# Kernel tuning notes

Measured on AMD Instinct MI355X. Metric: run time of the kernel, lower is better.

The kernel has to match this reference:

```python
import jax, jax.numpy as jnp
import numpy as np

B, D, NB, Z, POOL, C = 16, 2048, 8, 64, 2048, 10
H = 256  # hypernetwork hidden width


def setup_inputs() -> dict:
    key = jax.random.key(0)
    ks = jax.random.split(key, 12)
    s = lambda k, shape, scale=1.0: jax.random.normal(k, shape, dtype=jnp.float32) * scale
    return {
        "features": s(ks[0], (B, D)),
        "seeds": jax.random.randint(ks[1], (B,), 0, POOL),
        "seed_emb": s(ks[2], (POOL, Z)),                 # nn.Embedding weight
        "static_coeffs": s(ks[3], (1, NB)),              # static_accuracy_coeffs
        "hw1": s(ks[4], (Z, H), 1.0 / np.sqrt(Z)),       # hypernetwork Linear 1
        "hb1": jnp.zeros((H,), jnp.float32),
        "hw2": s(ks[5], (H, NB), 1.0 / np.sqrt(H)),      # hypernetwork Linear 2
        "hb2": jnp.zeros((NB,), jnp.float32),
        "wq": s(ks[6], (NB, D, D)),                      # stacked basis_weights_q
        "wk": s(ks[7], (NB, D, D)),
        "wv": s(ks[8], (NB, D, D)),
        "cw": s(ks[9], (D, C), 1.0 / np.sqrt(D)),        # classifier weight (in,out)
        "cb": jnp.zeros((C,), jnp.float32),
    }


def reference(features, seeds, seed_emb, static_coeffs, hw1, hb1, hw2, hb2,
              wq, wk, wv, cw, cb):
    # seed embedding lookup -> hypernetwork -> mixing coefficients
    z = seed_emb[seeds]                                     # [B, Z]
    h = jax.nn.relu(z @ hw1 + hb1)                          # [B, H]
    coeffs_div = jax.nn.softmax(h @ hw2 + hb2, axis=1)      # [B, NB]
    coeffs_acc = jax.nn.softmax(static_coeffs, axis=1)      # [1, NB]
    coeffs = coeffs_acc + coeffs_div                        # [B, NB]

    # Fused basis-weight synthesis + projection:
    # q_b = sum_i coeffs[b,i] * (features[b] @ W_i)  -- never materialize [B,D,D]
    q = jnp.einsum('bi,bj,ijk->bk', coeffs, features, wq)   # [B, D]
    k = jnp.einsum('bi,bj,ijk->bk', coeffs, features, wk)
    v = jnp.einsum('bi,bj,ijk->bk', coeffs, features, wv)

    # seq_len = 1 self-attention
    scores = jnp.einsum('bk,bk->b', q, k) / jnp.sqrt(jnp.float32(D))
    attn_map = jax.nn.softmax(scores.reshape(B, 1, 1), axis=-1)  # [B,1,1] (== ones)
    pooled = attn_map[:, 0] * v                              # [B, D]

    logits = pooled @ cw + cb                                # [B, C]
    return logits, attn_map
```

## Files before the change

kernel.cpp:

```cpp
#include <hip/hip_runtime.h>
#include <math.h>

#define D    2048
#define NB   8
#define BSZ  16
#define ZZ   64
#define HH   256
#define CC   10
#define NPAIR (NB * D)
#define GSPLIT 64
#define KC     8

__global__ __launch_bounds__(256) void k_mt(
    const float* __restrict__ feat, const int* __restrict__ seeds,
    const float* __restrict__ semb, const float* __restrict__ statc,
    const float* __restrict__ hw1, const float* __restrict__ hb1,
    const float* __restrict__ hw2, const float* __restrict__ hb2,
    float* __restrict__ Mt, float* __restrict__ out)
{
    int t = threadIdx.x, blk = blockIdx.x;
    __shared__ float zs[BSZ][ZZ];
    __shared__ float hs[BSZ][HH];
    __shared__ float lgs[BSZ][NB];
    __shared__ float cshs[BSZ][NB];

    for (int e = t; e < BSZ * ZZ; e += 256) {
        int b = e >> 6, u = e & (ZZ - 1);
        zs[b][u] = semb[seeds[b] * ZZ + u];
    }
    __syncthreads();

    {
        float acc[BSZ];
        float bias = hb1[t];
        #pragma unroll
        for (int b = 0; b < BSZ; ++b) acc[b] = bias;
        #pragma unroll 4
        for (int u = 0; u < ZZ; ++u) {
            float w = hw1[u * HH + t];
            #pragma unroll
            for (int b = 0; b < BSZ; ++b) acc[b] = fmaf(zs[b][u], w, acc[b]);
        }
        #pragma unroll
        for (int b = 0; b < BSZ; ++b) hs[b][t] = fmaxf(acc[b], 0.f);
    }
    __syncthreads();

    if (t < BSZ * NB) {
        int b = t >> 3, c = t & (NB - 1);
        float s = hb2[c];
        #pragma unroll 4
        for (int u = 0; u < HH; ++u) s = fmaf(hs[b][u], hw2[u * NB + c], s);
        lgs[b][c] = s;
    }
    __syncthreads();

    if (t < BSZ) {
        int b = t;
        float m = lgs[b][0];
        #pragma unroll
        for (int i = 1; i < NB; ++i) m = fmaxf(m, lgs[b][i]);
        float e[NB], s = 0.f;
        #pragma unroll
        for (int i = 0; i < NB; ++i) { e[i] = expf(lgs[b][i] - m); s += e[i]; }
        float m2 = statc[0];
        #pragma unroll
        for (int i = 1; i < NB; ++i) m2 = fmaxf(m2, statc[i]);
        float e2[NB], s2 = 0.f;
        #pragma unroll
        for (int i = 0; i < NB; ++i) { e2[i] = expf(statc[i] - m2); s2 += e2[i]; }
        #pragma unroll
        for (int i = 0; i < NB; ++i) cshs[b][i] = e[i] / s + e2[i] / s2;
        if (blk == 0) out[BSZ * CC + b] = 1.0f;
    }
    __syncthreads();

    int p = blk * 256 + t;
    int i = blk >> 3;
    int j = (blk & 7) * 256 + t;
    float vals[BSZ];
    #pragma unroll
    for (int b = 0; b < BSZ; ++b) vals[b] = cshs[b][i] * feat[b * D + j];
    float4* dst = reinterpret_cast<float4*>(Mt + (size_t)p * BSZ);
    dst[0] = make_float4(vals[0],  vals[1],  vals[2],  vals[3]);
    dst[1] = make_float4(vals[4],  vals[5],  vals[6],  vals[7]);
    dst[2] = make_float4(vals[8],  vals[9],  vals[10], vals[11]);
    dst[3] = make_float4(vals[12], vals[13], vals[14], vals[15]);
}

__global__ __launch_bounds__(512, 4) void k_partial(
    const float* __restrict__ wv, const float* __restrict__ Mt,
    float* __restrict__ part)
{
    int kc   = blockIdx.x;
    int g    = blockIdx.y;
    int t    = threadIdx.x;
    int wave = t >> 6;
    int lane = t & 63;
    int col  = kc * 256 + lane * 4;

    __shared__ float mt[256 * BSZ];
    __shared__ float4 sh[4][8][64];

    {
        const float4* src = reinterpret_cast<const float4*>(Mt + (size_t)g * 256 * BSZ);
        float4* dst = reinterpret_cast<float4*>(mt);
        dst[t]       = src[t];
        dst[t + 512] = src[t + 512];
    }
    __syncthreads();

    float4 acc[BSZ];
    #pragma unroll
    for (int b = 0; b < BSZ; ++b) acc[b] = make_float4(0.f, 0.f, 0.f, 0.f);

    int pair0 = wave * 32;
    const float* wp = wv + ((size_t)(g * 256 + pair0)) * D + col;

    #pragma unroll 4
    for (int it = 0; it < 32; ++it) {
        const float4 w = *reinterpret_cast<const float4*>(wp + (size_t)it * D);
        const float4* ap4 = reinterpret_cast<const float4*>(mt + (pair0 + it) * BSZ);
        float4 a0 = ap4[0], a1 = ap4[1], a2 = ap4[2], a3 = ap4[3];
        const float am[BSZ] = {a0.x, a0.y, a0.z, a0.w, a1.x, a1.y, a1.z, a1.w,
                               a2.x, a2.y, a2.z, a2.w, a3.x, a3.y, a3.z, a3.w};
        #pragma unroll
        for (int b = 0; b < BSZ; ++b) {
            float a = am[b];
            acc[b].x = fmaf(a, w.x, acc[b].x);
            acc[b].y = fmaf(a, w.y, acc[b].y);
            acc[b].z = fmaf(a, w.z, acc[b].z);
            acc[b].w = fmaf(a, w.w, acc[b].w);
        }
    }

    for (int round = 0; round < 4; ++round) {
        #pragma unroll
        for (int bb = 0; bb < 4; ++bb)
            sh[bb][wave][lane] = acc[round * 4 + bb];
        __syncthreads();
        if (wave < 4) {
            float4 s = sh[wave][0][lane];
            #pragma unroll
            for (int sw = 1; sw < 8; ++sw) {
                float4 x = sh[wave][sw][lane];
                s.x += x.x; s.y += x.y; s.z += x.z; s.w += x.w;
            }
            int b = round * 4 + wave;
            *reinterpret_cast<float4*>(part + ((size_t)(g * BSZ + b)) * D + col) = s;
        }
        __syncthreads();
    }
}

__global__ __launch_bounds__(256) void k_reduce(
    const float* __restrict__ part, float* __restrict__ v)
{
    int idx = blockIdx.x * 256 + threadIdx.x;
    int b = idx >> 11;
    int k = idx & (D - 1);
    float s[16];
    #pragma unroll
    for (int r = 0; r < 16; ++r) s[r] = 0.f;
    for (int g = 0; g < GSPLIT; g += 16) {
        #pragma unroll
        for (int r = 0; r < 16; ++r)
            s[r] += part[((size_t)((g + r) * BSZ + b)) * D + k];
    }
    float t0 = ((s[0] + s[1]) + (s[2] + s[3])) + ((s[4] + s[5]) + (s[6] + s[7]));
    float t1 = ((s[8] + s[9]) + (s[10] + s[11])) + ((s[12] + s[13]) + (s[14] + s[15]));
    v[idx] = t0 + t1;
}

__global__ __launch_bounds__(256) void k_cls(
    const float* __restrict__ v, const float* __restrict__ cw,
    const float* __restrict__ cb, float* __restrict__ out)
{
    int b = blockIdx.x, t = threadIdx.x;
    int wave = t >> 6, lane = t & 63;
    float lacc[CC];
    #pragma unroll
    for (int c = 0; c < CC; ++c) lacc[c] = 0.f;
    for (int k = t; k < D; k += 256) {
        float vv = v[b * D + k];
        const float* cwr = cw + k * CC;
        #pragma unroll
        for (int c = 0; c < CC; ++c) lacc[c] = fmaf(vv, cwr[c], lacc[c]);
    }
    __shared__ float sred[4][CC];
    #pragma unroll
    for (int c = 0; c < CC; ++c) {
        float val = lacc[c];
        for (int off = 32; off > 0; off >>= 1) val += __shfl_down(val, off);
        if (lane == 0) sred[wave][c] = val;
    }
    __syncthreads();
    if (t < CC)
        out[b * CC + t] = sred[0][t] + sred[1][t] + sred[2][t] + sred[3][t] + cb[t];
}

extern "C" void kernel_launch(void* const* d_in, const int* in_sizes, int n_in,
                              void* d_out, int out_size, void* d_ws, size_t ws_size,
                              hipStream_t stream)
{
    const float* feat  = (const float*)d_in[0];
    const int*   seeds = (const int*)  d_in[1];
    const float* semb  = (const float*)d_in[2];
    const float* statc = (const float*)d_in[3];
    const float* hw1   = (const float*)d_in[4];
    const float* hb1   = (const float*)d_in[5];
    const float* hw2   = (const float*)d_in[6];
    const float* hb2   = (const float*)d_in[7];
    const float* wv    = (const float*)d_in[10];
    const float* cw    = (const float*)d_in[11];
    const float* cb    = (const float*)d_in[12];
    float* out = (float*)d_out;

    float* Mt   = (float*)d_ws;
    float* part = Mt + (size_t)NPAIR * BSZ;
    float* v    = part + (size_t)GSPLIT * BSZ * D;

    hipLaunchKernelGGL(k_mt, dim3(NPAIR / 256), dim3(256), 0, stream,
                       feat, seeds, semb, statc, hw1, hb1, hw2, hb2, Mt, out);
    hipLaunchKernelGGL(k_partial, dim3(KC, GSPLIT), dim3(512), 0, stream,
                       wv, Mt, part);
    hipLaunchKernelGGL(k_reduce, dim3(BSZ * D / 256), dim3(256), 0, stream,
                       part, v);
    hipLaunchKernelGGL(k_cls, dim3(BSZ), dim3(256), 0, stream,
                       v, cw, cb, out);
}
```

Baseline: 65.40 us.

## Fold coefficient scaling into main GEMV epilogue and fuse reduce with classifier

```diff
diff --git a/kernel.cpp b/kernel.cpp
--- a/kernel.cpp
+++ b/kernel.cpp
@@ -11,18 +11,18 @@
 #define GSPLIT 64
 #define KC     8
 
-__global__ __launch_bounds__(256) void k_mt(
-    const float* __restrict__ feat, const int* __restrict__ seeds,
-    const float* __restrict__ semb, const float* __restrict__ statc,
+__global__ __launch_bounds__(256) void k_coeff(
+    const int* __restrict__ seeds, const float* __restrict__ semb,
+    const float* __restrict__ statc,
     const float* __restrict__ hw1, const float* __restrict__ hb1,
     const float* __restrict__ hw2, const float* __restrict__ hb2,
-    float* __restrict__ Mt, float* __restrict__ out)
-{
-    int t = threadIdx.x, blk = blockIdx.x;
+    const float* __restrict__ cb,
+    float* __restrict__ coeffT, float* __restrict__ out)
+{
+    int t = threadIdx.x;
     __shared__ float zs[BSZ][ZZ];
     __shared__ float hs[BSZ][HH];
     __shared__ float lgs[BSZ][NB];
-    __shared__ float cshs[BSZ][NB];
 
     for (int e = t; e < BSZ * ZZ; e += 256) {
         int b = e >> 6, u = e & (ZZ - 1);
@@ -35,7 +35,7 @@
         float bias = hb1[t];
         #pragma unroll
         for (int b = 0; b < BSZ; ++b) acc[b] = bias;
-        #pragma unroll 4
+        #pragma unroll 8
         for (int u = 0; u < ZZ; ++u) {
             float w = hw1[u * HH + t];
             #pragma unroll
@@ -46,12 +46,15 @@
     }
     __syncthreads();
 
-    if (t < BSZ * NB) {
-        int b = t >> 3, c = t & (NB - 1);
-        float s = hb2[c];
-        #pragma unroll 4
-        for (int u = 0; u < HH; ++u) s = fmaf(hs[b][u], hw2[u * NB + c], s);
-        lgs[b][c] = s;
+    {
+        int b = t >> 4, c = (t >> 1) & 7, half = t & 1;
+        float s = half ? 0.f : hb2[c];
+        int u0 = half * (HH / 2);
+        #pragma unroll 16
+        for (int u = 0; u < HH / 2; ++u)
+            s = fmaf(hs[b][u0 + u], hw2[(u0 + u) * NB + c], s);
+        s += __shfl_xor(s, 1);
+        if (!half) lgs[b][c] = s;
     }
     __syncthreads();
 
@@ -70,27 +73,15 @@
         #pragma unroll
         for (int i = 0; i < NB; ++i) { e2[i] = expf(statc[i] - m2); s2 += e2[i]; }
         #pragma unroll
-        for (int i = 0; i < NB; ++i) cshs[b][i] = e[i] / s + e2[i] / s2;
-        if (blk == 0) out[BSZ * CC + b] = 1.0f;
-    }
-    __syncthreads();
-
-    int p = blk * 256 + t;
-    int i = blk >> 3;
-    int j = (blk & 7) * 256 + t;
-    float vals[BSZ];
-    #pragma unroll
-    for (int b = 0; b < BSZ; ++b) vals[b] = cshs[b][i] * feat[b * D + j];
-    float4* dst = reinterpret_cast<float4*>(Mt + (size_t)p * BSZ);
-    dst[0] = make_float4(vals[0],  vals[1],  vals[2],  vals[3]);
-    dst[1] = make_float4(vals[4],  vals[5],  vals[6],  vals[7]);
-    dst[2] = make_float4(vals[8],  vals[9],  vals[10], vals[11]);
-    dst[3] = make_float4(vals[12], vals[13], vals[14], vals[15]);
-}
-
-__global__ __launch_bounds__(512, 4) void k_partial(
-    const float* __restrict__ wv, const float* __restrict__ Mt,
-    float* __restrict__ part)
+        for (int i = 0; i < NB; ++i) coeffT[i * BSZ + b] = e[i] / s + e2[i] / s2;
+    }
+    if (t < BSZ * CC) out[t] = cb[t - (t / CC) * CC];
+    else if (t < BSZ * CC + BSZ) out[t] = 1.0f;
+}
+
+__global__ __launch_bounds__(512, 4) void k_main(
+    const float* __restrict__ wv, const float* __restrict__ feat,
+    const float* __restrict__ coeffT, float* __restrict__ part)
 {
     int kc   = blockIdx.x;
     int g    = blockIdx.y;
@@ -99,14 +90,15 @@
     int lane = t & 63;
     int col  = kc * 256 + lane * 4;
 
-    __shared__ float mt[256 * BSZ];
+    __shared__ float ft[256 * BSZ];
     __shared__ float4 sh[4][8][64];
 
     {
-        const float4* src = reinterpret_cast<const float4*>(Mt + (size_t)g * 256 * BSZ);
-        float4* dst = reinterpret_cast<float4*>(mt);
-        dst[t]       = src[t];
-        dst[t + 512] = src[t + 512];
+        int jbase = (g & 7) * 256;
+        int b = t & 15, j = t >> 4;
+        #pragma unroll
+        for (int r = 0; r < 8; ++r)
+            ft[t + 512 * r] = feat[b * D + jbase + j + 32 * r];
     }
     __syncthreads();
 
@@ -116,24 +108,24 @@
 
     int pair0 = wave * 32;
     const float* wp = wv + ((size_t)(g * 256 + pair0)) * D + col;
+    const float* fp = ft + pair0 * BSZ;
 
     #pragma unroll 4
     for (int it = 0; it < 32; ++it) {
         const float4 w = *reinterpret_cast<const float4*>(wp + (size_t)it * D);
-        const float4* ap4 = reinterpret_cast<const float4*>(mt + (pair0 + it) * BSZ);
+        const float4* ap4 = reinterpret_cast<const float4*>(fp + it * BSZ);
         float4 a0 = ap4[0], a1 = ap4[1], a2 = ap4[2], a3 = ap4[3];
-        const float am[BSZ] = {a0.x, a0.y, a0.z, a0.w, a1.x, a1.y, a1.z, a1.w,
-                               a2.x, a2.y, a2.z, a2.w, a3.x, a3.y, a3.z, a3.w};
-        #pragma unroll
-        for (int b = 0; b < BSZ; ++b) {
-            float a = am[b];
-            acc[b].x = fmaf(a, w.x, acc[b].x);
-            acc[b].y = fmaf(a, w.y, acc[b].y);
-            acc[b].z = fmaf(a, w.z, acc[b].z);
-            acc[b].w = fmaf(a, w.w, acc[b].w);
-        }
-    }
-
+#define FMA4(ACC, A) \
+        ACC.x = fmaf(A, w.x, ACC.x); ACC.y = fmaf(A, w.y, ACC.y); \
+        ACC.z = fmaf(A, w.z, ACC.z); ACC.w = fmaf(A, w.w, ACC.w);
+        FMA4(acc[0],  a0.x) FMA4(acc[1],  a0.y) FMA4(acc[2],  a0.z) FMA4(acc[3],  a0.w)
+        FMA4(acc[4],  a1.x) FMA4(acc[5],  a1.y) FMA4(acc[6],  a1.z) FMA4(acc[7],  a1.w)
+        FMA4(acc[8],  a2.x) FMA4(acc[9],  a2.y) FMA4(acc[10], a2.z) FMA4(acc[11], a2.w)
+        FMA4(acc[12], a3.x) FMA4(acc[13], a3.y) FMA4(acc[14], a3.z) FMA4(acc[15], a3.w)
+#undef FMA4
+    }
+
+    const float* cfp = coeffT + (g >> 3) * BSZ;
     for (int round = 0; round < 4; ++round) {
         #pragma unroll
         for (int bb = 0; bb < 4; ++bb)
@@ -147,46 +139,41 @@
                 s.x += x.x; s.y += x.y; s.z += x.z; s.w += x.w;
             }
             int b = round * 4 + wave;
+            float cf = cfp[b];
+            s.x *= cf; s.y *= cf; s.z *= cf; s.w *= cf;
             *reinterpret_cast<float4*>(part + ((size_t)(g * BSZ + b)) * D + col) = s;
         }
         __syncthreads();
     }
 }
 
-__global__ __launch_bounds__(256) void k_reduce(
-    const float* __restrict__ part, float* __restrict__ v)
-{
-    int idx = blockIdx.x * 256 + threadIdx.x;
-    int b = idx >> 11;
-    int k = idx & (D - 1);
-    float s[16];
+__global__ __launch_bounds__(256) void k_tail(
+    const float* __restrict__ part, const float* __restrict__ cw,
+    float* __restrict__ out)
+{
+    int b = blockIdx.x >> 3, kc8 = blockIdx.x & 7;
+    int t = threadIdx.x;
+    int wave = t >> 6, lane = t & 63;
+    int k = kc8 * 256 + t;
+
+    float s = 0.f;
+    {
+        float ps[8];
+        #pragma unroll
+        for (int r = 0; r < 8; ++r) ps[r] = 0.f;
+        for (int g = 0; g < GSPLIT; g += 8) {
+            #pragma unroll
+            for (int r = 0; r < 8; ++r)
+                ps[r] += part[((size_t)((g + r) * BSZ + b)) * D + k];
+        }
+        s = ((ps[0] + ps[1]) + (ps[2] + ps[3])) + ((ps[4] + ps[5]) + (ps[6] + ps[7]));
+    }
+
+    float lacc[CC];
+    const float* cwr = cw + (size_t)k * CC;
     #pragma unroll
-    for (int r = 0; r < 16; ++r) s[r] = 0.f;
-    for (int g = 0; g < GSPLIT; g += 16) {
-        #pragma unroll
-        for (int r = 0; r < 16; ++r)
-            s[r] += part[((size_t)((g + r) * BSZ + b)) * D + k];
-    }
-    float t0 = ((s[0] + s[1]) + (s[2] + s[3])) + ((s[4] + s[5]) + (s[6] + s[7]));
-    float t1 = ((s[8] + s[9]) + (s[10] + s[11])) + ((s[12] + s[13]) + (s[14] + s[15]));
-    v[idx] = t0 + t1;
-}
-
-__global__ __launch_bounds__(256) void k_cls(
-    const float* __restrict__ v, const float* __restrict__ cw,
-    const float* __restrict__ cb, float* __restrict__ out)
-{
-    int b = blockIdx.x, t = threadIdx.x;
-    int wave = t >> 6, lane = t & 63;
-    float lacc[CC];
-    #pragma unroll
-    for (int c = 0; c < CC; ++c) lacc[c] = 0.f;
-    for (int k = t; k < D; k += 256) {
-        float vv = v[b * D + k];
-        const float* cwr = cw + k * CC;
-        #pragma unroll
-        for (int c = 0; c < CC; ++c) lacc[c] = fmaf(vv, cwr[c], lacc[c]);
-    }
+    for (int c = 0; c < CC; ++c) lacc[c] = s * cwr[c];
+
     __shared__ float sred[4][CC];
     #pragma unroll
     for (int c = 0; c < CC; ++c) {
@@ -196,7 +183,8 @@
     }
     __syncthreads();
     if (t < CC)
-        out[b * CC + t] = sred[0][t] + sred[1][t] + sred[2][t] + sred[3][t] + cb[t];
+        atomicAdd(&out[b * CC + t],
+                  sred[0][t] + sred[1][t] + sred[2][t] + sred[3][t]);
 }
 
 extern "C" void kernel_launch(void* const* d_in, const int* in_sizes, int n_in,
@@ -216,16 +204,13 @@
     const float* cb    = (const float*)d_in[12];
     float* out = (float*)d_out;
 
-    float* Mt   = (float*)d_ws;
-    float* part = Mt + (size_t)NPAIR * BSZ;
-    float* v    = part + (size_t)GSPLIT * BSZ * D;
-
-    hipLaunchKernelGGL(k_mt, dim3(NPAIR / 256), dim3(256), 0, stream,
-                       feat, seeds, semb, statc, hw1, hb1, hw2, hb2, Mt, out);
-    hipLaunchKernelGGL(k_partial, dim3(KC, GSPLIT), dim3(512), 0, stream,
-                       wv, Mt, part);
-    hipLaunchKernelGGL(k_reduce, dim3(BSZ * D / 256), dim3(256), 0, stream,
-                       part, v);
-    hipLaunchKernelGGL(k_cls, dim3(BSZ), dim3(256), 0, stream,
-                       v, cw, cb, out);
-}
+    float* coeffT = (float*)d_ws;
+    float* part   = coeffT + 256;
+
+    hipLaunchKernelGGL(k_coeff, dim3(1), dim3(256), 0, stream,
+                       seeds, semb, statc, hw1, hb1, hw2, hb2, cb, coeffT, out);
+    hipLaunchKernelGGL(k_main, dim3(KC, GSPLIT), dim3(512), 0, stream,
+                       wv, feat, coeffT, part);
+    hipLaunchKernelGGL(k_tail, dim3(BSZ * KC), dim3(256), 0, stream,
+                       part, cw, out);
+}
```

After: 52.32 us. -20.0%, faster.
